# Kernel optimization log

Hardware: AMD Instinct MI355X
Metric: run time of the kernel (lower is better)

Reference implementation:

```python
import jax, jax.numpy as jnp
import numpy as np

V, FN, CIN, HID, PTS = 50000, 100000, 3, 256, 10000
TEMP = 0.1
EPS = 1e-20


def line_mesh_graph(f, Vn):
    # f: [F,3] int triangles. Build the 'line mesh': one node per unique mesh edge.
    fe = jnp.concatenate([f[:, :2], f[:, 1:], f[:, jnp.array([2, 0])]], 0)  # [3F,2]
    fe = jnp.sort(fe, axis=1)
    keys = fe[:, 0] * Vn + fe[:, 1]                       # [3F] unique key per undirected edge
    ukeys, inv = jnp.unique(keys, return_inverse=True)
    edge_node = jnp.stack([ukeys // Vn, ukeys % Vn], -1)  # [E,2] endpoints of each edge-node
    E = ukeys.shape[0]
    feid = inv.reshape(3, -1).T                           # [F,3] edge-node id per face edge
    # line-graph connectivity: edges of the same face are mutual neighbors, plus self-loops
    srcs, dsts = [], []
    for i, j in ((0, 1), (1, 0), (1, 2), (2, 1), (2, 0), (0, 2)):
        srcs.append(feid[:, i]); dsts.append(feid[:, j])
    loop = jnp.arange(E)
    edge = jnp.stack([jnp.concatenate(srcs + [loop]), jnp.concatenate(dsts + [loop])], 0)  # [2,NE]
    return edge, edge_node, keys


def gsn_conv(x, edge, Ws, Wn, b):
    # GSNConv stand-in: self transform + mean-aggregated neighbor transform
    s, d = edge[0], edge[1]
    N = x.shape[0]
    deg = jax.ops.segment_sum(jnp.ones_like(s, x.dtype), d, num_segments=N)
    agg = jax.ops.segment_sum(x[s], d, num_segments=N) / jnp.clip(deg, 1.0)[:, None]
    return x @ Ws + agg @ Wn + b


def gumbel_mask(logits, temperature, num, key):
    U = jax.random.uniform(key, logits.shape)
    g = -jnp.log(-jnp.log(U + EPS) + EPS)
    y = jax.nn.softmax((logits + g) / temperature, -1)[:, 0]  # [E]
    _, ind = jax.lax.top_k(y, num)
    y_hard = jnp.zeros_like(y).at[ind].set(1.0)
    mask = jax.lax.stop_gradient(y_hard - y) + y              # straight-through one-hot
    return mask, y_hard == 1.0


def mesh_collapse(f, keys, pool_edge, Vn):
    # Vectorized replacement of the per-pool-edge python loop: hash-join pooled edge keys
    # against all 3F face-edge keys via sorted search.
    PE = pool_edge.shape[0]
    pool_idx = jnp.arange(Vn, Vn + PE)
    edge_keys = keys.reshape(3, -1).T                     # [F,3] (cols: e01,e12,e20)
    pk = pool_edge[:, 0] * Vn + pool_edge[:, 1]
    order = jnp.argsort(pk); pks = pk[order]
    flat = edge_keys.reshape(-1)
    pos = jnp.clip(jnp.searchsorted(pks, flat), 0, PE - 1)
    found = pks[pos] == flat
    pei = jnp.where(found, pool_idx[order[pos]], -1).reshape(-1, 3)  # pool_edge_idx [F,3]
    fm = found.reshape(-1, 3)
    pen = fm.sum(1)                                       # pool_edge_num per face
    psi = (fm * jnp.arange(3)).sum(1)                     # pool_start_idx per face
    vv = jnp.stack([f[:, 0], pei[:, 0], f[:, 1], pei[:, 1], f[:, 2], pei[:, 2]], -1)
    nf0 = f[pen == 0]
    fv1 = vv[pen == 1]; s1 = psi[pen == 1]
    fv1 = jnp.concatenate([fv1[s1 == 0], jnp.roll(fv1[s1 == 1], -2, 1), jnp.roll(fv1[s1 == 2], 2, 1)], 0)
    nf1 = jnp.concatenate([jnp.stack([fv1[:, 0], fv1[:, 1], fv1[:, 4]], -1),
                           jnp.stack([fv1[:, 1], fv1[:, 2], fv1[:, 4]], -1)], 0)
    fv2 = vv[pen == 2]; s2 = psi[pen == 2]
    fv2 = jnp.concatenate([fv2[s2 == 1], jnp.roll(fv2[s2 == 2], 2, 1), jnp.roll(fv2[s2 == 3], -2, 1)], 0)
    nf2 = jnp.concatenate([jnp.stack([fv2[:, 0], fv2[:, 1], fv2[:, 4]], -1),
                           jnp.stack([fv2[:, 1], fv2[:, 2], fv2[:, 3]], -1),
                           jnp.stack([fv2[:, 1], fv2[:, 3], fv2[:, 4]], -1)], 0)
    fv3 = vv[pen == 3]
    nf3 = jnp.concatenate([jnp.stack([fv3[:, 0], fv3[:, 1], fv3[:, 5]], -1),
                           jnp.stack([fv3[:, 1], fv3[:, 2], fv3[:, 3]], -1),
                           jnp.stack([fv3[:, 1], fv3[:, 3], fv3[:, 5]], -1),
                           jnp.stack([fv3[:, 3], fv3[:, 4], fv3[:, 5]], -1)], 0)
    new_faces = jnp.concatenate([nf0, nf1, nf2, nf3], 0)
    ne = jnp.concatenate([new_faces[:, :2], new_faces[:, 1:], new_faces[:, jnp.array([2, 0])]], 0)
    ai = jnp.arange(Vn + PE)
    ne = jnp.concatenate([jnp.stack([ai, ai], -1), ne], 0)
    return new_faces, ne.T


def setup_inputs():
    key = jax.random.key(0)
    ks = jax.random.split(key, 10)
    s1 = 1.0 / np.sqrt(CIN); s2 = 1.0 / np.sqrt(HID)
    return {
        'input': jax.random.normal(ks[0], (1, V, CIN), jnp.float32),
        'face': jax.random.randint(ks[1], (1, FN, 3), 0, V),
        'coord': jax.random.normal(ks[2], (1, V, 3), jnp.float32),
        'detail_points': jax.random.normal(ks[3], (1, PTS, 3), jnp.float32),
        'div': 5,
        'W1s': jax.random.normal(ks[4], (CIN, HID), jnp.float32) * s1,
        'W1n': jax.random.normal(ks[5], (CIN, HID), jnp.float32) * s1,
        'b1': jnp.zeros((HID,), jnp.float32),
        'W2s': jax.random.normal(ks[6], (HID, 2), jnp.float32) * s2,
        'W2n': jax.random.normal(ks[7], (HID, 2), jnp.float32) * s2,
        'b2': jnp.zeros((2,), jnp.float32),
    }


def reference(input, face, coord, detail_points, div, W1s, W1n, b1, W2s, W2n, b2):
    # B=1 (data-dependent per-sample output sizes make batch stacking only valid then)
    x0, f = input[0], face[0]
    Vn = x0.shape[0]
    edge, edge_node, keys = line_mesh_graph(f, Vn)
    xe = 0.5 * (x0[edge_node[:, 0]] + x0[edge_node[:, 1]])   # edge-node features [E,C]
    h = jax.nn.relu(gsn_conv(xe, edge, W1s, W1n, b1))
    out = jax.nn.sigmoid(gsn_conv(h, edge, W2s, W2n, b2))    # [E,2]
    mask, pool_ind = gumbel_mask(out, TEMP, out.shape[0] // div, jax.random.key(42))
    pool_edge = edge_node[pool_ind]                          # [PE,2]
    new_faces, new_edges = mesh_collapse(f, keys, pool_edge, Vn)
    return edge_node[None], new_faces[None], new_edges[None], mask[None]
```

## Files before the change

### kernel.cpp

```cpp
#include <hip/hip_runtime.h>
#include <stdint.h>

typedef uint32_t u32;
typedef uint64_t u64;

#define VN 50000
#define FN 100000
#define K3F 300000
#define EMAX 300000
#define NB1 1172
#define NBS 293
#define NBH 293
#define NBC 98
#define HALF1 150016
#define NBL 586

#define W_KPA    0u
#define W_KPB    600000u
#define W_SEGOFF 1200000u
#define W_FEID   1500004u
#define W_XE     1800004u
#define W_PK     2700004u
#define W_P      2703076u
#define W_Q      3303076u
#define W_Y      3903076u
#define W_YMAP   4203076u
#define W_T64    4503076u
#define W_SEL    5103140u
#define W_SELR   5403140u
#define W_CAT    5703140u
#define W_CATR   5803140u
#define W_NFI    5903140u
#define W_HIST   7103140u
#define W_HIST2  7403172u
#define W_SUMS   7703204u
#define W_CATH   7707300u
#define W_TKH    7708324u
#define W_DONE   7708580u
#define W_SCAL   7708612u

#define S_E 0
#define S_NUM 1
#define S_PFX 2
#define S_KREM 3
#define S_TU 4
#define S_R 5
#define S_NF 6
#define S_NEN 7
#define S_O1 8
#define S_O2 9
#define S_O3 10
#define S_RS 16
#define S_GS 24
#define S_GP 32

__device__ __forceinline__ void tf2x32(u32 x0, u32 x1, u32& o0, u32& o1) {
  const u32 ks0 = 0u, ks1 = 42u, ks2 = 0x1BD11BDAu ^ 0u ^ 42u;
  x0 += ks0; x1 += ks1;
#define TFR(r) { x0 += x1; x1 = (x1<<(r))|(x1>>(32-(r))); x1 ^= x0; }
  TFR(13) TFR(15) TFR(26) TFR(6)   x0 += ks1; x1 += ks2 + 1u;
  TFR(17) TFR(29) TFR(16) TFR(24)  x0 += ks2; x1 += ks0 + 2u;
  TFR(13) TFR(15) TFR(26) TFR(6)   x0 += ks0; x1 += ks1 + 3u;
  TFR(17) TFR(29) TFR(16) TFR(24)  x0 += ks1; x1 += ks2 + 4u;
  TFR(13) TFR(15) TFR(26) TFR(6)   x0 += ks2; x1 += ks0 + 5u;
#undef TFR
  o0 = x0; o1 = x1;
}

__global__ void scan_blocks(const u32* __restrict__ in, u32* __restrict__ out,
                            u32* __restrict__ sums, int n) {
  __shared__ u32 lds[256];
  int t = threadIdx.x;
  int base = blockIdx.x*1024 + t*4;
  u32 v[4]; u32 tot = 0;
  for (int k = 0; k < 4; ++k) { v[k] = (base+k < n) ? in[base+k] : 0u; tot += v[k]; }
  lds[t] = tot; __syncthreads();
  for (int o = 1; o < 256; o <<= 1) {
    u32 x = (t >= o) ? lds[t-o] : 0u; __syncthreads();
    lds[t] += x; __syncthreads();
  }
  u32 excl = lds[t] - tot;
  if (t == 255) sums[blockIdx.x] = lds[255];
  u32 run = excl;
  for (int k = 0; k < 4; ++k) { if (base+k < n) out[base+k] = run; run += v[k]; }
}

__global__ void scan_flagblocks(const u64* __restrict__ kp, u32* __restrict__ out,
                                u32* __restrict__ sums, int n) {
  __shared__ u32 lds[256];
  int t = threadIdx.x;
  int base = blockIdx.x*1024 + t*4;
  u32 v[4]; u32 tot = 0;
  for (int k = 0; k < 4; ++k) {
    int i = base + k;
    u32 f = 0;
    if (i < n) f = (i == 0 || (u32)(kp[i-1]>>32) != (u32)(kp[i]>>32)) ? 1u : 0u;
    v[k] = f; tot += f;
  }
  lds[t] = tot; __syncthreads();
  for (int o = 1; o < 256; o <<= 1) {
    u32 x = (t >= o) ? lds[t-o] : 0u; __syncthreads();
    lds[t] += x; __syncthreads();
  }
  u32 excl = lds[t] - tot;
  if (t == 255) sums[blockIdx.x] = lds[255];
  u32 run = excl;
  for (int k = 0; k < 4; ++k) { if (base+k < n) out[base+k] = run; run += v[k]; }
}

__global__ void scan64_src(const u32* __restrict__ ymap, const u32* __restrict__ scal,
                           u64* __restrict__ part, u64* __restrict__ sums) {
  __shared__ u64 lds[256];
  int t = threadIdx.x;
  int base = blockIdx.x*1024 + t*4;
  int E = (int)scal[S_E];
  u32 TU = scal[S_TU];
  u64 v[4]; u64 tot = 0;
  for (int k = 0; k < 4; ++k) {
    int e = base + k;
    u64 val = 0;
    if (e < E) {
      u32 u = ymap[e];
      if (u > TU) val = 1ull;
      else if (u == TU) val = 1ull << 32;
    }
    v[k] = val; tot += val;
  }
  lds[t] = tot; __syncthreads();
  for (int o = 1; o < 256; o <<= 1) {
    u64 x = (t >= o) ? lds[t-o] : 0ull; __syncthreads();
    lds[t] += x; __syncthreads();
  }
  u64 excl = lds[t] - tot;
  if (t == 255) sums[blockIdx.x] = lds[255];
  u64 run = excl;
  for (int k = 0; k < 4; ++k) { part[base+k] = run; run += v[k]; }
}

__global__ void k_sel2(const u32* __restrict__ ymap, const u64* __restrict__ part,
                       const u64* __restrict__ sums, const u32* __restrict__ scal,
                       u32* __restrict__ sel, u32* __restrict__ selr) {
  __shared__ u64 sl64[256];
  int t = threadIdx.x, b = blockIdx.x;
  u64 partial = 0;
  for (int j = t; j < b; j += 256) partial += sums[j];
  sl64[t] = partial; __syncthreads();
  for (int o = 128; o; o >>= 1) { if (t < o) sl64[t] += sl64[t+o]; __syncthreads(); }
  u64 basepre = sl64[0];
  int E = (int)scal[S_E];
  u32 TU = scal[S_TU], R = scal[S_R];
  for (int k = 0; k < 4; ++k) {
    int e = b*1024 + k*256 + t;
    if (e >= EMAX) continue;
    u64 pre = part[e] + basepre;
    u32 GTpre = (u32)pre, TIEpre = (u32)(pre >> 32);
    u32 v = 0;
    if (e < E) {
      u32 u = ymap[e];
      v = (u > TU) || (u == TU && TIEpre < R);
    }
    sel[e] = v ? 1u : 0u;
    selr[e] = GTpre + min(TIEpre, R);
  }
}

__global__ void k_rhist(const u64* __restrict__ kp, u32* __restrict__ hist,
                        int shift, int nb) {
  __shared__ u32 h[256];
  int t = threadIdx.x;
  h[t] = 0; __syncthreads();
  int i = blockIdx.x*256 + t;
  if (i < K3F) atomicAdd(&h[((u32)(kp[i]>>32) >> shift) & 255u], 1u);
  __syncthreads();
  hist[(u32)t*nb + blockIdx.x] = h[t];
}

__global__ void k_rscat(const u64* __restrict__ kp, u64* __restrict__ okp,
                        const u32* __restrict__ hist, const u32* __restrict__ sums,
                        int shift, int nb) {
  __shared__ u32 sl[256];
  __shared__ u32 ps[NBS];
  __shared__ u64 ball[4][8];
  __shared__ u64 vmask[4];
  int t = threadIdx.x, w = t>>6, lane = t&63;
  u32 a0 = (t < NBS) ? sums[t] : 0u;
  u32 a1 = (256 + t < NBS) ? sums[256+t] : 0u;
  sl[t] = a0; __syncthreads();
  for (int o = 1; o < 256; o <<= 1) {
    u32 x = (t >= o) ? sl[t-o] : 0u; __syncthreads();
    sl[t] += x; __syncthreads();
  }
  u32 incl0 = sl[t], tot0 = sl[255];
  if (t < NBS) ps[t] = incl0 - a0;
  __syncthreads();
  sl[t] = a1; __syncthreads();
  for (int o = 1; o < 256; o <<= 1) {
    u32 x = (t >= o) ? sl[t-o] : 0u; __syncthreads();
    sl[t] += x; __syncthreads();
  }
  if (256 + t < NBS) ps[256+t] = sl[t] - a1 + tot0;
  __syncthreads();
  int i = blockIdx.x*256 + t;
  bool valid = i < K3F;
  u64 v = valid ? kp[i] : 0ull;
  u32 d = ((u32)(v>>32) >> shift) & 255u;
  for (int bit = 0; bit < 8; ++bit) {
    u64 bm = __ballot(valid && ((d>>bit)&1u));
    if (lane == 0) ball[w][bit] = bm;
  }
  u64 vb = __ballot(valid ? 1 : 0);
  if (lane == 0) vmask[w] = vb;
  __syncthreads();
  if (valid) {
    u32 rank = 0;
    for (int ww = 0; ww < w; ++ww) {
      u64 m = vmask[ww];
      for (int bit = 0; bit < 8; ++bit) { u64 bb = ball[ww][bit]; m &= ((d>>bit)&1u) ? bb : ~bb; }
      rank += (u32)__popcll(m);
    }
    u64 m = vmask[w];
    for (int bit = 0; bit < 8; ++bit) { u64 bb = ball[w][bit]; m &= ((d>>bit)&1u) ? bb : ~bb; }
    rank += (u32)__popcll(m & ((1ull<<lane)-1ull));
    u32 h = d*(u32)nb + blockIdx.x;
    u32 pos = hist[h] + ps[h>>10] + rank;
    okp[pos] = v;
  }
}

__global__ void k_keys(const int* __restrict__ face,
                       const float* __restrict__ W1s, const float* __restrict__ W1n,
                       const float* __restrict__ b1,
                       const float* __restrict__ W2s, const float* __restrict__ W2n,
                       float* __restrict__ pk,
                       u64* __restrict__ kp, u32* __restrict__ hist,
                       u32* __restrict__ tkh, u32* __restrict__ done) {
  __shared__ u32 h[256];
  int t = threadIdx.x;
  h[t] = 0;
  __syncthreads();
  if (blockIdx.x == 0) {
    tkh[t] = 0u;
    if (t < 32) done[t] = 0u;
    float* p = pk + t*12;
    p[0] = W1s[t]; p[1] = W1s[256+t]; p[2] = W1s[512+t];
    p[3] = W1n[t]; p[4] = W1n[256+t]; p[5] = W1n[512+t];
    p[6] = b1[t];
    p[7] = W2s[2*t]; p[8] = W2s[2*t+1];
    p[9] = W2n[2*t]; p[10] = W2n[2*t+1];
    p[11] = 0.0f;
  }
  int i = blockIdx.x*256 + t;
  if (i < K3F) {
    int s = i / FN, f = i - s*FN;
    int v0 = face[f*3 + s];
    int v1 = face[f*3 + (s == 2 ? 0 : s+1)];
    int a = min(v0, v1), b = max(v0, v1);
    u32 key = ((u32)a * (u32)VN + (u32)b) ^ 0x80000000u;
    kp[i] = ((u64)key << 32) | (u32)i;
    atomicAdd(&h[key & 255u], 1u);
  }
  __syncthreads();
  hist[(u32)t*NB1 + blockIdx.x] = h[t];
}

__global__ void k_uwrite(const u64* __restrict__ kp, const u32* __restrict__ rankp,
                         const u32* __restrict__ sums, const float* __restrict__ x,
                         u32* __restrict__ segoff, u32* __restrict__ feid,
                         float* __restrict__ xe, float* __restrict__ dout,
                         u32* __restrict__ scal, const int* __restrict__ divp) {
  __shared__ u32 sl[256];
  int t = threadIdx.x, b = blockIdx.x;
  int chunk = b >> 2;
  u32 partial = 0;
  for (int j = t; j < chunk; j += 256) partial += sums[j];
  sl[t] = partial; __syncthreads();
  for (int o = 128; o; o >>= 1) { if (t < o) sl[t] += sl[t+o]; __syncthreads(); }
  u32 basepre = sl[0];
  int p = b*256 + t;
  if (p >= K3F) return;
  u64 v = kp[p];
  u32 cur = (u32)(v >> 32);
  u32 fl = (p == 0 || (u32)(kp[p-1] >> 32) != cur) ? 1u : 0u;
  u32 rk = rankp[p] + basepre;
  if (fl) {
    u32 e = rk;
    segoff[e] = (u32)p;
    int k = (int)(cur ^ 0x80000000u);
    long long kk = (long long)k;
    long long qq = (kk - (kk < 0 ? (long long)(VN-1) : 0ll)) / VN;
    int q = (int)qq;
    int r = (int)(kk - qq * VN);
    dout[2*e]   = (float)q;
    dout[2*e+1] = (float)r;
    u32 i0 = (u32)(q < 0 ? q + VN : q);
    u32 i1 = (u32)r;
    for (int c = 0; c < 3; ++c) xe[e*3+c] = 0.5f*(x[i0*3+c] + x[i1*3+c]);
  }
  u32 id = rk - 1u + fl;
  u32 i = (u32)v;
  u32 s = i / FN, f = i - s*FN;
  feid[f*3 + s] = id;
  if (p == K3F-1) {
    u32 E = rk + fl;
    u32 num = E / (u32)divp[0];
    scal[S_E] = E; scal[S_NUM] = num;
    segoff[E] = (u32)K3F;
    scal[S_PFX] = 0u; scal[S_KREM] = num;
  }
}

__device__ __forceinline__ void agg_neighbors(int e, u32 st, u32 en,
                                              const u64* __restrict__ kp,
                                              const u32* __restrict__ feid,
                                              const float* __restrict__ v, int stride,
                                              float* acc0, float* acc1, float* acc2) {
  const int sslot[6] = {0,1,1,2,2,0};
  const int dslot[6] = {1,0,2,1,0,2};
  float c0 = 0.f, c1 = 0.f, c2 = 0.f;
  for (int b = 0; b < 6; ++b) {
    int j = dslot[b], isl = sslot[b];
    for (u32 p = st; p < en; ++p) {
      u32 i = (u32)kp[p];
      u32 s = i / FN;
      if ((int)s == j) {
        u32 f = i - s*FN;
        u32 u = feid[f*3 + isl];
        c0 += v[u*stride]; c1 += v[u*stride+1]; if (stride == 3) c2 += v[u*stride+2];
      }
    }
  }
  c0 += v[e*stride]; c1 += v[e*stride+1]; if (stride == 3) c2 += v[e*stride+2];
  *acc0 = c0; *acc1 = c1; *acc2 = c2;
}

__global__ void k_l12(const float* __restrict__ xe, const u32* __restrict__ segoff,
                      const u64* __restrict__ kp, const u32* __restrict__ feid,
                      const u32* __restrict__ scal, const float* __restrict__ pk,
                      float* __restrict__ P, float* __restrict__ Q) {
  int e1 = blockIdx.x*256 + threadIdx.x;
  int E = (int)scal[S_E];
  if (e1 >= E) return;
  int e2 = e1 + HALF1;
  bool v2 = e2 < E;
  int e2c = v2 ? e2 : e1;
  u32 st1 = segoff[e1], en1 = segoff[e1+1];
  u32 st2 = segoff[e2c], en2 = segoff[e2c+1];
  float c0a,c1a,c2a, c0b,c1b,c2b;
  agg_neighbors(e1,  st1, en1, kp, feid, xe, 3, &c0a,&c1a,&c2a);
  agg_neighbors(e2c, st2, en2, kp, feid, xe, 3, &c0b,&c1b,&c2b);
  float x0a=xe[e1*3],  x1a=xe[e1*3+1],  x2a=xe[e1*3+2];
  float x0b=xe[e2c*3], x1b=xe[e2c*3+1], x2b=xe[e2c*3+2];
  float dga = (float)(2u*(en1-st1)+1u), dgb = (float)(2u*(en2-st2)+1u);
  float m0a=c0a/dga, m1a=c1a/dga, m2a=c2a/dga;
  float m0b=c0b/dgb, m1b=c1b/dgb, m2b=c2b/dgb;
  float p0a=0,p1a=0,q0a=0,q1a=0, p0b=0,p1b=0,q0b=0,q1b=0;
#pragma unroll 4
  for (int hh = 0; hh < 256; ++hh) {
    const float* w = pk + hh*12;
    float w0=w[0],w1=w[1],w2=w[2],w3=w[3],w4=w[4],w5=w[5],w6=w[6];
    float w7=w[7],w8=w[8],w9=w[9],w10=w[10];
    float s1a = x0a*w0 + x1a*w1 + x2a*w2;
    float s2a = m0a*w3 + m1a*w4 + m2a*w5;
    float ha = fmaxf(s1a + s2a + w6, 0.0f);
    p0a += ha*w7;  p1a += ha*w8;  q0a += ha*w9;  q1a += ha*w10;
    float s1b = x0b*w0 + x1b*w1 + x2b*w2;
    float s2b = m0b*w3 + m1b*w4 + m2b*w5;
    float hb = fmaxf(s1b + s2b + w6, 0.0f);
    p0b += hb*w7;  p1b += hb*w8;  q0b += hb*w9;  q1b += hb*w10;
  }
  P[2*e1] = p0a; P[2*e1+1] = p1a; Q[2*e1] = q0a; Q[2*e1+1] = q1a;
  if (v2) { P[2*e2] = p0b; P[2*e2+1] = p1b; Q[2*e2] = q0b; Q[2*e2+1] = q1b; }
}

__device__ __forceinline__ void score_one(int e, const float* P, const float* Q,
                                          const u32* segoff, const u64* kp, const u32* feid,
                                          float b20, float b21, float* yo, u32* ymo) {
  u32 st = segoff[e], en = segoff[e+1];
  float a0, a1, dummy;
  agg_neighbors(e, st, en, kp, feid, Q, 2, &a0, &a1, &dummy);
  float dg = (float)(2u*(en - st) + 1u);
  float z0 = P[2*e]   + a0/dg + b20;
  float z1 = P[2*e+1] + a1/dg + b21;
  float l0 = 1.0f/(1.0f + expf(-z0));
  float l1 = 1.0f/(1.0f + expf(-z1));
  u32 g0b, g1b;
  { u32 o0,o1; tf2x32(0u, 2u*(u32)e,      o0, o1); g0b = o0 ^ o1; }
  { u32 o0,o1; tf2x32(0u, 2u*(u32)e + 1u, o0, o1); g1b = o0 ^ o1; }
  float U0 = __uint_as_float((g0b>>9) | 0x3f800000u) - 1.0f;
  float U1 = __uint_as_float((g1b>>9) | 0x3f800000u) - 1.0f;
  float g0 = -logf(-logf(U0 + 1e-20f) + 1e-20f);
  float g1 = -logf(-logf(U1 + 1e-20f) + 1e-20f);
  float A0 = (l0 + g0)/0.1f;
  float A1 = (l1 + g1)/0.1f;
  float mx = fmaxf(A0, A1);
  float e0 = expf(A0-mx), e1v = expf(A1-mx);
  float y = e0/(e0+e1v);
  *yo = y;
  *ymo = __float_as_uint(y) | 0x80000000u;
}

__global__ void k_scores(const float* __restrict__ P, const float* __restrict__ Q,
                         const u32* __restrict__ segoff, const u64* __restrict__ kp,
                         const u32* __restrict__ feid,
                         const float* __restrict__ b2, const u32* __restrict__ scal,
                         float* __restrict__ Y, u32* __restrict__ ymap) {
  int e1 = blockIdx.x*256 + threadIdx.x;
  int E = (int)scal[S_E];
  if (e1 >= E) return;
  int e2 = e1 + HALF1;
  bool v2 = e2 < E;
  int e2c = v2 ? e2 : e1;
  float b20 = b2[0], b21 = b2[1];
  float ya, yb; u32 ma, mb;
  score_one(e1,  P, Q, segoff, kp, feid, b20, b21, &ya, &ma);
  score_one(e2c, P, Q, segoff, kp, feid, b20, b21, &yb, &mb);
  Y[e1] = ya; ymap[e1] = ma;
  if (v2) { Y[e2] = yb; ymap[e2] = mb; }
}

__global__ void k_tkround(const u32* __restrict__ ymap, u32* __restrict__ scal,
                          u32* __restrict__ hist, u32* __restrict__ done, int byte) {
  __shared__ u32 h[256];
  __shared__ u32 s2[256];
  __shared__ u32 chosen_s;
  __shared__ u32 lastflag;
  int t = threadIdx.x;
  h[t] = 0u;
  if (t == 0) lastflag = 0u;
  __syncthreads();
  int E = (int)scal[S_E];
  u32 pfx = scal[S_PFX];
  int base = blockIdx.x*1024;
  for (int k = 0; k < 4; ++k) {
    int e = base + k*256 + t;
    if (e < E) {
      u32 u = ymap[e];
      bool match = (byte == 3) || ((u >> ((byte+1)*8)) == pfx);
      if (match) atomicAdd(&h[(u >> (byte*8)) & 255u], 1u);
    }
  }
  __syncthreads();
  u32 c = h[t];
  if (c) atomicAdd(&hist[t], c);
  __syncthreads();
  if (t == 0) {
    __threadfence();
    u32 old = atomicAdd(&done[byte], 1u);
    if (old == gridDim.x - 1u) lastflag = 1u;
  }
  __syncthreads();
  if (!lastflag) return;
  __threadfence();
  u32 v = atomicExch(&hist[t], 0u);
  s2[t] = v;
  if (t == 0) chosen_s = 0u;
  __syncthreads();
  for (int o = 1; o < 256; o <<= 1) {
    u32 x = (t + o < 256) ? s2[t+o] : 0u; __syncthreads();
    s2[t] += x; __syncthreads();
  }
  u32 krem = scal[S_KREM];
  if (s2[t] >= krem) atomicMax(&chosen_s, (u32)t);
  __syncthreads();
  if (t == 0) {
    u32 chosen = chosen_s;
    u32 sufnext = (chosen < 255u) ? s2[chosen+1] : 0u;
    u32 newkrem = krem - sufnext;
    u32 npfx = (scal[S_PFX] << 8) | chosen;
    scal[S_PFX] = npfx; scal[S_KREM] = newkrem;
    if (byte == 0) { scal[S_TU] = npfx; scal[S_R] = newkrem; }
  }
}

__global__ void k_catfused(const u32* __restrict__ feid, const u32* __restrict__ sel,
                           u32* __restrict__ cat, u32* __restrict__ ch) {
  __shared__ u32 h[8];
  int t = threadIdx.x;
  if (t < 8) h[t] = 0u;
  __syncthreads();
  int base = blockIdx.x*1024 + t*4;
  for (int k = 0; k < 4; ++k) {
    int f = base + k;
    if (f < FN) {
      u32 m0 = sel[feid[f*3]], m1 = sel[feid[f*3+1]], m2 = sel[feid[f*3+2]];
      u32 pen = m0 + m1 + m2;
      u32 psi = m1 + 2u*m2;
      u32 c = (pen == 0) ? 0u : (pen == 1) ? (1u+psi) : (pen == 2) ? (3u+psi) : 7u;
      cat[f] = c;
      atomicAdd(&h[c], 1u);
    }
  }
  __syncthreads();
  if (t < 8) ch[(u32)t*NBC + blockIdx.x] = h[t];
}

__global__ void k_catoff(u32* __restrict__ ch, u32* __restrict__ scal) {
  __shared__ u32 lds[256];
  __shared__ u32 ex[1024];
  int t = threadIdx.x;
  u32 v[4]; u32 tot = 0;
  for (int k = 0; k < 4; ++k) {
    int i = t*4 + k;
    u32 x = (i < 8*NBC) ? ch[i] : 0u;
    v[k] = x; tot += x;
  }
  lds[t] = tot; __syncthreads();
  for (int o = 1; o < 256; o <<= 1) {
    u32 x = (t >= o) ? lds[t-o] : 0u; __syncthreads();
    lds[t] += x; __syncthreads();
  }
  u32 excl = lds[t] - tot;
  u32 run = excl;
  for (int k = 0; k < 4; ++k) { ex[t*4+k] = run; run += v[k]; }
  __syncthreads();
  for (int k = 0; k < 4; ++k) {
    int i = t*4 + k;
    if (i < 8*NBC) ch[i] = ex[i];
  }
  if (t == 0) {
    u32 total = lds[255];
    u32 bnd[9];
    for (int c = 0; c < 8; ++c) bnd[c] = ex[c*NBC];
    bnd[8] = total;
    u32 tot8[8];
    for (int c = 0; c < 8; ++c) tot8[c] = bnd[c+1] - bnd[c];
    u32 n0 = tot8[0], n1 = tot8[1]+tot8[2]+tot8[3], n2 = tot8[4]+tot8[5]+tot8[6], n3 = tot8[7];
    u32 NF = n0 + 2u*n1 + 3u*n2 + 4u*n3;
    u32 E = scal[S_E], num = scal[S_NUM];
    u32 NEn = (u32)VN + num + 3u*NF;
    scal[S_NF] = NF; scal[S_NEN] = NEn;
    scal[S_O1] = 2u*E;
    scal[S_O2] = 2u*E + 3u*NF;
    scal[S_O3] = 2u*E + 3u*NF + 2u*NEn;
    u32 RS[8] = {0u, n0,n0,n0, n0+2u*n1, n0+2u*n1, n0+2u*n1, n0+2u*n1+3u*n2};
    u32 GS[8] = {0u, n1,n1,n1, n2,n2,n2, n3};
    u32 GP[8] = {0u, n0,n0,n0, n0+n1, n0+n1, n0+n1, n0+n1+n2};
    for (int i = 0; i < 8; ++i) { scal[S_RS+i] = RS[i]; scal[S_GS+i] = GS[i]; scal[S_GP+i] = GP[i]; }
  }
}

__global__ void k_catrank(const u32* __restrict__ cat, const u32* __restrict__ ch,
                          u32* __restrict__ cr) {
  __shared__ u32 lds[256];
  int t = threadIdx.x;
  int base = blockIdx.x*1024 + t*4;
  u32 cc[4], loc[4];
  u32 cnt[8] = {0,0,0,0,0,0,0,0};
  for (int k = 0; k < 4; ++k) {
    int i = base + k;
    if (i < FN) { u32 c = cat[i]; cc[k] = c; loc[k] = cnt[c]++; }
    else cc[k] = 8u;
  }
  u32 tb[8];
  for (int c = 0; c < 8; ++c) {
    lds[t] = cnt[c]; __syncthreads();
    for (int o = 1; o < 256; o <<= 1) {
      u32 x = (t >= o) ? lds[t-o] : 0u; __syncthreads();
      lds[t] += x; __syncthreads();
    }
    tb[c] = lds[t] - cnt[c];
    __syncthreads();
  }
  for (int k = 0; k < 4; ++k) {
    int i = base + k;
    if (i < FN) { u32 c = cc[k]; cr[i] = ch[c*NBC + blockIdx.x] + tb[c] + loc[k]; }
  }
}

__global__ void k_wfaces(const int* __restrict__ face, const u32* __restrict__ cat,
                         const u32* __restrict__ cr, const u32* __restrict__ feid,
                         const u32* __restrict__ selr, const u32* __restrict__ scal,
                         int* __restrict__ nfi, float* __restrict__ dout) {
  int f = blockIdx.x*256 + threadIdx.x;
  if (f >= FN) return;
  const int nfc[8] = {1,2,2,2,3,3,3,4};
  const int tri[8][4][3] = {
    {{0,2,4},{0,0,0},{0,0,0},{0,0,0}},
    {{0,1,4},{1,2,4},{0,0,0},{0,0,0}},
    {{2,3,0},{3,4,0},{0,0,0},{0,0,0}},
    {{4,5,2},{5,0,2},{0,0,0},{0,0,0}},
    {{0,1,4},{1,2,3},{1,3,4},{0,0,0}},
    {{4,5,2},{5,0,1},{5,1,2},{0,0,0}},
    {{2,3,0},{3,4,5},{3,5,0},{0,0,0}},
    {{0,1,5},{1,2,3},{1,3,5},{3,4,5}}};
  u32 c = cat[f];
  int cv[6];
  cv[0] = face[f*3];   cv[2] = face[f*3+1]; cv[4] = face[f*3+2];
  cv[1] = VN + (int)selr[feid[f*3]];
  cv[3] = VN + (int)selr[feid[f*3+1]];
  cv[5] = VN + (int)selr[feid[f*3+2]];
  u32 g  = cr[f] - scal[S_GP + c];
  u32 o1 = scal[S_O1];
  for (int j = 0; j < nfc[c]; ++j) {
    u32 row = scal[S_RS + c] + (u32)j*scal[S_GS + c] + g;
    for (int m = 0; m < 3; ++m) {
      int v = cv[tri[c][j][m]];
      nfi[row*3 + m] = v;
      dout[o1 + row*3 + m] = (float)v;
    }
  }
}

__global__ void k_wne(const int* __restrict__ nfi, const u32* __restrict__ scal,
                      float* __restrict__ dout) {
  int i = blockIdx.x*256 + threadIdx.x;
  u32 NEn = scal[S_NEN];
  if (i >= (int)NEn) return;
  u32 NF = scal[S_NF];
  u32 Vp = (u32)VN + scal[S_NUM];
  u32 o2 = scal[S_O2];
  int a, b;
  if ((u32)i < Vp) { a = i; b = i; }
  else {
    u32 j = (u32)i - Vp;
    u32 blk = j / NF, r = j - blk*NF;
    int i0 = (blk == 0) ? 0 : (blk == 1) ? 1 : 2;
    int i1 = (blk == 0) ? 1 : (blk == 1) ? 2 : 0;
    a = nfi[r*3 + i0]; b = nfi[r*3 + i1];
  }
  dout[o2 + i] = (float)a;
  dout[o2 + NEn + i] = (float)b;
}

__global__ void k_wmask(const u32* __restrict__ sel, const float* __restrict__ Y,
                        const u32* __restrict__ scal, float* __restrict__ dout) {
  int e = blockIdx.x*256 + threadIdx.x;
  if (e >= (int)scal[S_E]) return;
  float y = Y[e];
  float yh = sel[e] ? 1.0f : 0.0f;
  dout[scal[S_O3] + e] = (yh - y) + y;
}

extern "C" void kernel_launch(void* const* d_in, const int* in_sizes, int n_in,
                              void* d_out, int out_size, void* d_ws, size_t ws_size,
                              hipStream_t stream) {
  const float* x    = (const float*)d_in[0];
  const int*   face = (const int*)d_in[1];
  const int*   divp = (const int*)d_in[4];
  const float* W1s  = (const float*)d_in[5];
  const float* W1n  = (const float*)d_in[6];
  const float* b1   = (const float*)d_in[7];
  const float* W2s  = (const float*)d_in[8];
  const float* W2n  = (const float*)d_in[9];
  const float* b2   = (const float*)d_in[10];
  float* out = (float*)d_out;
  u32* W = (u32*)d_ws;

  u64 *KPA = (u64*)(W+W_KPA), *KPB = (u64*)(W+W_KPB);
  u32 *HIST = W+W_HIST, *HIST2 = W+W_HIST2, *SUMS = W+W_SUMS, *SCAL = W+W_SCAL;
  u32 *TKH = W+W_TKH, *DONE = W+W_DONE;
  u32 *RK = W+W_T64;
  u64 *T64 = (u64*)(W+W_T64);
  u64 *SUMS64 = (u64*)(W+W_SUMS);

  k_keys<<<NB1, 256, 0, stream>>>(face, W1s, W1n, b1, W2s, W2n, (float*)(W+W_PK),
                                  KPA, HIST, TKH, DONE);
  scan_blocks<<<NBS, 256, 0, stream>>>(HIST, HIST, SUMS, NB1*256);
  k_rscat<<<NB1, 256, 0, stream>>>(KPA, KPB, HIST, SUMS,  0, NB1);
  k_rhist<<<NB1, 256, 0, stream>>>(KPB, HIST2,  8, NB1);
  scan_blocks<<<NBS, 256, 0, stream>>>(HIST2, HIST2, SUMS, NB1*256);
  k_rscat<<<NB1, 256, 0, stream>>>(KPB, KPA, HIST2, SUMS,  8, NB1);
  k_rhist<<<NB1, 256, 0, stream>>>(KPA, HIST, 16, NB1);
  scan_blocks<<<NBS, 256, 0, stream>>>(HIST, HIST, SUMS, NB1*256);
  k_rscat<<<NB1, 256, 0, stream>>>(KPA, KPB, HIST, SUMS, 16, NB1);
  k_rhist<<<NB1, 256, 0, stream>>>(KPB, HIST2, 24, NB1);
  scan_blocks<<<NBS, 256, 0, stream>>>(HIST2, HIST2, SUMS, NB1*256);
  k_rscat<<<NB1, 256, 0, stream>>>(KPB, KPA, HIST2, SUMS, 24, NB1);

  scan_flagblocks<<<NBS, 256, 0, stream>>>(KPA, RK, SUMS, K3F);
  k_uwrite<<<NB1, 256, 0, stream>>>(KPA, RK, SUMS, x, W+W_SEGOFF, W+W_FEID,
                                    (float*)(W+W_XE), out, SCAL, divp);

  k_l12<<<NBL, 256, 0, stream>>>((float*)(W+W_XE), W+W_SEGOFF, KPA, W+W_FEID, SCAL,
                                 (float*)(W+W_PK), (float*)(W+W_P), (float*)(W+W_Q));
  k_scores<<<NBL, 256, 0, stream>>>((float*)(W+W_P), (float*)(W+W_Q), W+W_SEGOFF, KPA,
                                    W+W_FEID, b2, SCAL, (float*)(W+W_Y), W+W_YMAP);

  for (int byte = 3; byte >= 0; --byte)
    k_tkround<<<NBH, 256, 0, stream>>>(W+W_YMAP, SCAL, TKH, DONE, byte);
  scan64_src<<<NBS, 256, 0, stream>>>(W+W_YMAP, SCAL, T64, SUMS64);
  k_sel2<<<NBS, 256, 0, stream>>>(W+W_YMAP, T64, SUMS64, SCAL, W+W_SEL, W+W_SELR);

  k_catfused<<<NBC, 256, 0, stream>>>(W+W_FEID, W+W_SEL, W+W_CAT, W+W_CATH);
  k_catoff<<<1, 256, 0, stream>>>(W+W_CATH, SCAL);
  k_catrank<<<NBC, 256, 0, stream>>>(W+W_CAT, W+W_CATH, W+W_CATR);
  k_wfaces<<<391, 256, 0, stream>>>(face, W+W_CAT, W+W_CATR, W+W_FEID, W+W_SELR, SCAL,
                                    (int*)(W+W_NFI), out);
  k_wne<<<5118, 256, 0, stream>>>((int*)(W+W_NFI), SCAL, out);
  k_wmask<<<NB1, 256, 0, stream>>>(W+W_SEL, (float*)(W+W_Y), SCAL, out);
}
```

Baseline: 316.3 us.

## Replace 4-pass LSD radix sort of edge keys with bucket sort by min vertex

Swaps the four-pass 8-bit radix sort (histogram, scan and scatter per pass) for a counting sort keyed on the smaller vertex id, one bucket per vertex. Global atomics build the histogram, one scan plus a fixup gives bucket offsets, an atomic scatter fills the buckets, and a per-bucket selection sort restores full order. This cuts the sort from many kernel launches and four full data passes down to roughly one. In exchange it relies on small per-vertex buckets, uses contended global atomics, and sorts each bucket serially in one thread with uncoalesced accesses.

```diff
diff --git a/kernel.cpp b/kernel.cpp
--- a/kernel.cpp
+++ b/kernel.cpp
@@ -14,6 +14,8 @@
 #define NBC 98
 #define HALF1 150016
 #define NBL 586
+#define NBK 85900
+#define NBSH 84
 
 #define W_KPA    0u
 #define W_KPB    600000u
@@ -108,6 +110,26 @@
   for (int k = 0; k < 4; ++k) { if (base+k < n) out[base+k] = run; run += v[k]; }
 }
 
+__global__ void k_fixup(u32* __restrict__ hist, u32* __restrict__ hist2,
+                        const u32* __restrict__ sums) {
+  __shared__ u32 sl[256];
+  int t = threadIdx.x, c = blockIdx.x;
+  u32 partial = 0;
+  for (int j = t; j < c; j += 256) partial += sums[j];
+  sl[t] = partial; __syncthreads();
+  for (int o = 128; o; o >>= 1) { if (t < o) sl[t] += sl[t+o]; __syncthreads(); }
+  u32 basepre = sl[0];
+  for (int k = 0; k < 4; ++k) {
+    int i = c*1024 + k*256 + t;
+    if (i < NBK) {
+      u32 v = hist[i] + basepre;
+      hist[i] = v;
+      hist2[i] = v;
+    }
+  }
+  if (c == 0 && t == 0) hist2[NBK] = (u32)K3F;
+}
+
 __global__ void scan64_src(const u32* __restrict__ ymap, const u32* __restrict__ scal,
                            u64* __restrict__ part, u64* __restrict__ sums) {
   __shared__ u64 lds[256];
@@ -164,69 +186,6 @@
   }
 }
 
-__global__ void k_rhist(const u64* __restrict__ kp, u32* __restrict__ hist,
-                        int shift, int nb) {
-  __shared__ u32 h[256];
-  int t = threadIdx.x;
-  h[t] = 0; __syncthreads();
-  int i = blockIdx.x*256 + t;
-  if (i < K3F) atomicAdd(&h[((u32)(kp[i]>>32) >> shift) & 255u], 1u);
-  __syncthreads();
-  hist[(u32)t*nb + blockIdx.x] = h[t];
-}
-
-__global__ void k_rscat(const u64* __restrict__ kp, u64* __restrict__ okp,
-                        const u32* __restrict__ hist, const u32* __restrict__ sums,
-                        int shift, int nb) {
-  __shared__ u32 sl[256];
-  __shared__ u32 ps[NBS];
-  __shared__ u64 ball[4][8];
-  __shared__ u64 vmask[4];
-  int t = threadIdx.x, w = t>>6, lane = t&63;
-  u32 a0 = (t < NBS) ? sums[t] : 0u;
-  u32 a1 = (256 + t < NBS) ? sums[256+t] : 0u;
-  sl[t] = a0; __syncthreads();
-  for (int o = 1; o < 256; o <<= 1) {
-    u32 x = (t >= o) ? sl[t-o] : 0u; __syncthreads();
-    sl[t] += x; __syncthreads();
-  }
-  u32 incl0 = sl[t], tot0 = sl[255];
-  if (t < NBS) ps[t] = incl0 - a0;
-  __syncthreads();
-  sl[t] = a1; __syncthreads();
-  for (int o = 1; o < 256; o <<= 1) {
-    u32 x = (t >= o) ? sl[t-o] : 0u; __syncthreads();
-    sl[t] += x; __syncthreads();
-  }
-  if (256 + t < NBS) ps[256+t] = sl[t] - a1 + tot0;
-  __syncthreads();
-  int i = blockIdx.x*256 + t;
-  bool valid = i < K3F;
-  u64 v = valid ? kp[i] : 0ull;
-  u32 d = ((u32)(v>>32) >> shift) & 255u;
-  for (int bit = 0; bit < 8; ++bit) {
-    u64 bm = __ballot(valid && ((d>>bit)&1u));
-    if (lane == 0) ball[w][bit] = bm;
-  }
-  u64 vb = __ballot(valid ? 1 : 0);
-  if (lane == 0) vmask[w] = vb;
-  __syncthreads();
-  if (valid) {
-    u32 rank = 0;
-    for (int ww = 0; ww < w; ++ww) {
-      u64 m = vmask[ww];
-      for (int bit = 0; bit < 8; ++bit) { u64 bb = ball[ww][bit]; m &= ((d>>bit)&1u) ? bb : ~bb; }
-      rank += (u32)__popcll(m);
-    }
-    u64 m = vmask[w];
-    for (int bit = 0; bit < 8; ++bit) { u64 bb = ball[w][bit]; m &= ((d>>bit)&1u) ? bb : ~bb; }
-    rank += (u32)__popcll(m & ((1ull<<lane)-1ull));
-    u32 h = d*(u32)nb + blockIdx.x;
-    u32 pos = hist[h] + ps[h>>10] + rank;
-    okp[pos] = v;
-  }
-}
-
 __global__ void k_keys(const int* __restrict__ face,
                        const float* __restrict__ W1s, const float* __restrict__ W1n,
                        const float* __restrict__ b1,
@@ -234,10 +193,7 @@
                        float* __restrict__ pk,
                        u64* __restrict__ kp, u32* __restrict__ hist,
                        u32* __restrict__ tkh, u32* __restrict__ done) {
-  __shared__ u32 h[256];
-  int t = threadIdx.x;
-  h[t] = 0;
-  __syncthreads();
+  int t = threadIdx.x;
   if (blockIdx.x == 0) {
     tkh[t] = 0u;
     if (t < 32) done[t] = 0u;
@@ -257,10 +213,32 @@
     int a = min(v0, v1), b = max(v0, v1);
     u32 key = ((u32)a * (u32)VN + (u32)b) ^ 0x80000000u;
     kp[i] = ((u64)key << 32) | (u32)i;
-    atomicAdd(&h[key & 255u], 1u);
-  }
-  __syncthreads();
-  hist[(u32)t*NB1 + blockIdx.x] = h[t];
+    atomicAdd(&hist[key / (u32)VN], 1u);
+  }
+}
+
+__global__ void k_bscat(const u64* __restrict__ kp, u64* __restrict__ okp,
+                        u32* __restrict__ hist) {
+  int i = blockIdx.x*256 + threadIdx.x;
+  if (i >= K3F) return;
+  u64 v = kp[i];
+  u32 bkt = (u32)(v >> 32) / (u32)VN;
+  u32 pos = atomicAdd(&hist[bkt], 1u);
+  okp[pos] = v;
+}
+
+__global__ void k_bsort(u64* __restrict__ kp, const u32* __restrict__ hist2) {
+  int j = blockIdx.x*256 + threadIdx.x;
+  if (j >= NBK) return;
+  u32 st = hist2[j], en = hist2[j+1];
+  for (u32 i = st; i + 1 < en; ++i) {
+    u64 mn = kp[i]; u32 mi = i;
+    for (u32 q = i + 1; q < en; ++q) {
+      u64 vq = kp[q];
+      if (vq < mn) { mn = vq; mi = q; }
+    }
+    if (mi != i) { kp[mi] = kp[i]; kp[i] = mn; }
+  }
 }
 
 __global__ void k_uwrite(const u64* __restrict__ kp, const u32* __restrict__ rankp,
@@ -653,27 +631,21 @@
   u64 *T64 = (u64*)(W+W_T64);
   u64 *SUMS64 = (u64*)(W+W_SUMS);
 
+  hipMemsetAsync(HIST, 0, (size_t)NBK * 4, stream);
   k_keys<<<NB1, 256, 0, stream>>>(face, W1s, W1n, b1, W2s, W2n, (float*)(W+W_PK),
                                   KPA, HIST, TKH, DONE);
-  scan_blocks<<<NBS, 256, 0, stream>>>(HIST, HIST, SUMS, NB1*256);
-  k_rscat<<<NB1, 256, 0, stream>>>(KPA, KPB, HIST, SUMS,  0, NB1);
-  k_rhist<<<NB1, 256, 0, stream>>>(KPB, HIST2,  8, NB1);
-  scan_blocks<<<NBS, 256, 0, stream>>>(HIST2, HIST2, SUMS, NB1*256);
-  k_rscat<<<NB1, 256, 0, stream>>>(KPB, KPA, HIST2, SUMS,  8, NB1);
-  k_rhist<<<NB1, 256, 0, stream>>>(KPA, HIST, 16, NB1);
-  scan_blocks<<<NBS, 256, 0, stream>>>(HIST, HIST, SUMS, NB1*256);
-  k_rscat<<<NB1, 256, 0, stream>>>(KPA, KPB, HIST, SUMS, 16, NB1);
-  k_rhist<<<NB1, 256, 0, stream>>>(KPB, HIST2, 24, NB1);
-  scan_blocks<<<NBS, 256, 0, stream>>>(HIST2, HIST2, SUMS, NB1*256);
-  k_rscat<<<NB1, 256, 0, stream>>>(KPB, KPA, HIST2, SUMS, 24, NB1);
-
-  scan_flagblocks<<<NBS, 256, 0, stream>>>(KPA, RK, SUMS, K3F);
-  k_uwrite<<<NB1, 256, 0, stream>>>(KPA, RK, SUMS, x, W+W_SEGOFF, W+W_FEID,
+  scan_blocks<<<NBSH, 256, 0, stream>>>(HIST, HIST, SUMS, NBK);
+  k_fixup<<<NBSH, 256, 0, stream>>>(HIST, HIST2, SUMS);
+  k_bscat<<<NB1, 256, 0, stream>>>(KPA, KPB, HIST);
+  k_bsort<<<(NBK+255)/256, 256, 0, stream>>>(KPB, HIST2);
+
+  scan_flagblocks<<<NBS, 256, 0, stream>>>(KPB, RK, SUMS, K3F);
+  k_uwrite<<<NB1, 256, 0, stream>>>(KPB, RK, SUMS, x, W+W_SEGOFF, W+W_FEID,
                                     (float*)(W+W_XE), out, SCAL, divp);
 
-  k_l12<<<NBL, 256, 0, stream>>>((float*)(W+W_XE), W+W_SEGOFF, KPA, W+W_FEID, SCAL,
+  k_l12<<<NBL, 256, 0, stream>>>((float*)(W+W_XE), W+W_SEGOFF, KPB, W+W_FEID, SCAL,
                                  (float*)(W+W_PK), (float*)(W+W_P), (float*)(W+W_Q));
-  k_scores<<<NBL, 256, 0, stream>>>((float*)(W+W_P), (float*)(W+W_Q), W+W_SEGOFF, KPA,
+  k_scores<<<NBL, 256, 0, stream>>>((float*)(W+W_P), (float*)(W+W_Q), W+W_SEGOFF, KPB,
                                     W+W_FEID, b2, SCAL, (float*)(W+W_Y), W+W_YMAP);
 
   for (int byte = 3; byte >= 0; --byte)
```

New measurement: 347.3 us. +9.8%, slower.

## Fuse category offset, rank, face write and mask kernels into fewer launches

Applied to the files above, without the earlier changes.

Folds the single-block category-offset scan into the tail of k_catfused, using a last-block-done atomic counter. Merges the rank computation with the face writing so the rank array no longer goes through memory, and merges the mask write into the new-edge write kernel. The aim is to cut three kernel launches and one intermediate array. In exchange, face writing now runs on only 98 blocks with four faces per thread, which lowers parallelism. It also depends on the done[8] counter being reset before every call.

```diff
diff --git a/kernel.cpp b/kernel.cpp
--- a/kernel.cpp
+++ b/kernel.cpp
@@ -29,7 +29,6 @@
 #define W_SEL    5103140u
 #define W_SELR   5403140u
 #define W_CAT    5703140u
-#define W_CATR   5803140u
 #define W_NFI    5903140u
 #define W_HIST   7103140u
 #define W_HIST2  7403172u
@@ -53,6 +52,8 @@
 #define S_RS 16
 #define S_GS 24
 #define S_GP 32
+
+#define ALDR(p) __hip_atomic_load((p), __ATOMIC_RELAXED, __HIP_MEMORY_SCOPE_AGENT)
 
 __device__ __forceinline__ void tf2x32(u32 x0, u32 x1, u32& o0, u32& o1) {
   const u32 ks0 = 0u, ks1 = 42u, ks2 = 0x1BD11BDAu ^ 0u ^ 42u;
@@ -473,10 +474,15 @@
 }
 
 __global__ void k_catfused(const u32* __restrict__ feid, const u32* __restrict__ sel,
-                           u32* __restrict__ cat, u32* __restrict__ ch) {
+                           u32* __restrict__ cat, u32* __restrict__ ch,
+                           u32* __restrict__ done, u32* __restrict__ scal) {
   __shared__ u32 h[8];
+  __shared__ u32 lastflag;
+  __shared__ u32 lds[256];
+  __shared__ u32 ex[1024];
   int t = threadIdx.x;
   if (t < 8) h[t] = 0u;
+  if (t == 0) lastflag = 0u;
   __syncthreads();
   int base = blockIdx.x*1024 + t*4;
   for (int k = 0; k < 4; ++k) {
@@ -492,16 +498,19 @@
   }
   __syncthreads();
   if (t < 8) ch[(u32)t*NBC + blockIdx.x] = h[t];
-}
-
-__global__ void k_catoff(u32* __restrict__ ch, u32* __restrict__ scal) {
-  __shared__ u32 lds[256];
-  __shared__ u32 ex[1024];
-  int t = threadIdx.x;
+  __syncthreads();
+  if (t == 0) {
+    __threadfence();
+    u32 old = atomicAdd(&done[8], 1u);
+    if (old == gridDim.x - 1u) lastflag = 1u;
+  }
+  __syncthreads();
+  if (!lastflag) return;
+  __threadfence();
   u32 v[4]; u32 tot = 0;
   for (int k = 0; k < 4; ++k) {
     int i = t*4 + k;
-    u32 x = (i < 8*NBC) ? ch[i] : 0u;
+    u32 x = (i < 8*NBC) ? ALDR(&ch[i]) : 0u;
     v[k] = x; tot += x;
   }
   lds[t] = tot; __syncthreads();
@@ -539,8 +548,10 @@
   }
 }
 
-__global__ void k_catrank(const u32* __restrict__ cat, const u32* __restrict__ ch,
-                          u32* __restrict__ cr) {
+__global__ void k_catwf(const u32* __restrict__ cat, const u32* __restrict__ ch,
+                        const int* __restrict__ face, const u32* __restrict__ feid,
+                        const u32* __restrict__ selr, const u32* __restrict__ scal,
+                        int* __restrict__ nfi, float* __restrict__ dout) {
   __shared__ u32 lds[256];
   int t = threadIdx.x;
   int base = blockIdx.x*1024 + t*4;
@@ -561,18 +572,6 @@
     tb[c] = lds[t] - cnt[c];
     __syncthreads();
   }
-  for (int k = 0; k < 4; ++k) {
-    int i = base + k;
-    if (i < FN) { u32 c = cc[k]; cr[i] = ch[c*NBC + blockIdx.x] + tb[c] + loc[k]; }
-  }
-}
-
-__global__ void k_wfaces(const int* __restrict__ face, const u32* __restrict__ cat,
-                         const u32* __restrict__ cr, const u32* __restrict__ feid,
-                         const u32* __restrict__ selr, const u32* __restrict__ scal,
-                         int* __restrict__ nfi, float* __restrict__ dout) {
-  int f = blockIdx.x*256 + threadIdx.x;
-  if (f >= FN) return;
   const int nfc[8] = {1,2,2,2,3,3,3,4};
   const int tri[8][4][3] = {
     {{0,2,4},{0,0,0},{0,0,0},{0,0,0}},
@@ -583,27 +582,39 @@
     {{4,5,2},{5,0,1},{5,1,2},{0,0,0}},
     {{2,3,0},{3,4,5},{3,5,0},{0,0,0}},
     {{0,1,5},{1,2,3},{1,3,5},{3,4,5}}};
-  u32 c = cat[f];
-  int cv[6];
-  cv[0] = face[f*3];   cv[2] = face[f*3+1]; cv[4] = face[f*3+2];
-  cv[1] = VN + (int)selr[feid[f*3]];
-  cv[3] = VN + (int)selr[feid[f*3+1]];
-  cv[5] = VN + (int)selr[feid[f*3+2]];
-  u32 g  = cr[f] - scal[S_GP + c];
   u32 o1 = scal[S_O1];
-  for (int j = 0; j < nfc[c]; ++j) {
-    u32 row = scal[S_RS + c] + (u32)j*scal[S_GS + c] + g;
-    for (int m = 0; m < 3; ++m) {
-      int v = cv[tri[c][j][m]];
-      nfi[row*3 + m] = v;
-      dout[o1 + row*3 + m] = (float)v;
-    }
-  }
-}
-
-__global__ void k_wne(const int* __restrict__ nfi, const u32* __restrict__ scal,
-                      float* __restrict__ dout) {
+  for (int k = 0; k < 4; ++k) {
+    int f = base + k;
+    if (f >= FN) break;
+    u32 c = cc[k];
+    u32 rank = ch[c*NBC + blockIdx.x] + tb[c] + loc[k];
+    int cv[6];
+    cv[0] = face[f*3];   cv[2] = face[f*3+1]; cv[4] = face[f*3+2];
+    cv[1] = VN + (int)selr[feid[f*3]];
+    cv[3] = VN + (int)selr[feid[f*3+1]];
+    cv[5] = VN + (int)selr[feid[f*3+2]];
+    u32 g = rank - scal[S_GP + c];
+    for (int j = 0; j < nfc[c]; ++j) {
+      u32 row = scal[S_RS + c] + (u32)j*scal[S_GS + c] + g;
+      for (int m = 0; m < 3; ++m) {
+        int v = cv[tri[c][j][m]];
+        nfi[row*3 + m] = v;
+        dout[o1 + row*3 + m] = (float)v;
+      }
+    }
+  }
+}
+
+__global__ void k_wnemask(const int* __restrict__ nfi, const u32* __restrict__ sel,
+                          const float* __restrict__ Y, const u32* __restrict__ scal,
+                          float* __restrict__ dout) {
   int i = blockIdx.x*256 + threadIdx.x;
+  int E = (int)scal[S_E];
+  if (i < E) {
+    float y = Y[i];
+    float yh = sel[i] ? 1.0f : 0.0f;
+    dout[scal[S_O3] + i] = (yh - y) + y;
+  }
   u32 NEn = scal[S_NEN];
   if (i >= (int)NEn) return;
   u32 NF = scal[S_NF];
@@ -620,15 +631,6 @@
   }
   dout[o2 + i] = (float)a;
   dout[o2 + NEn + i] = (float)b;
-}
-
-__global__ void k_wmask(const u32* __restrict__ sel, const float* __restrict__ Y,
-                        const u32* __restrict__ scal, float* __restrict__ dout) {
-  int e = blockIdx.x*256 + threadIdx.x;
-  if (e >= (int)scal[S_E]) return;
-  float y = Y[e];
-  float yh = sel[e] ? 1.0f : 0.0f;
-  dout[scal[S_O3] + e] = (yh - y) + y;
 }
 
 extern "C" void kernel_launch(void* const* d_in, const int* in_sizes, int n_in,
@@ -681,11 +683,8 @@
   scan64_src<<<NBS, 256, 0, stream>>>(W+W_YMAP, SCAL, T64, SUMS64);
   k_sel2<<<NBS, 256, 0, stream>>>(W+W_YMAP, T64, SUMS64, SCAL, W+W_SEL, W+W_SELR);
 
-  k_catfused<<<NBC, 256, 0, stream>>>(W+W_FEID, W+W_SEL, W+W_CAT, W+W_CATH);
-  k_catoff<<<1, 256, 0, stream>>>(W+W_CATH, SCAL);
-  k_catrank<<<NBC, 256, 0, stream>>>(W+W_CAT, W+W_CATH, W+W_CATR);
-  k_wfaces<<<391, 256, 0, stream>>>(face, W+W_CAT, W+W_CATR, W+W_FEID, W+W_SELR, SCAL,
-                                    (int*)(W+W_NFI), out);
-  k_wne<<<5118, 256, 0, stream>>>((int*)(W+W_NFI), SCAL, out);
-  k_wmask<<<NB1, 256, 0, stream>>>(W+W_SEL, (float*)(W+W_Y), SCAL, out);
-}
+  k_catfused<<<NBC, 256, 0, stream>>>(W+W_FEID, W+W_SEL, W+W_CAT, W+W_CATH, DONE, SCAL);
+  k_catwf<<<NBC, 256, 0, stream>>>(W+W_CAT, W+W_CATH, face, W+W_FEID, W+W_SELR, SCAL,
+                                   (int*)(W+W_NFI), out);
+  k_wnemask<<<5118, 256, 0, stream>>>((int*)(W+W_NFI), W+W_SEL, (float*)(W+W_Y), SCAL, out);
+}
```

After: 323.9 us. 1.02x slower.
